# Kernel optimization log

Measured on AMD Instinct MI355X. Metric: run time of the kernel, lower is better.

The kernel has to match this reference:

```python
import jax, jax.numpy as jnp
import numpy as np

EPS = 1e-5

def _conv1x1(x, W, b):
    # x: [B,Ci,H,W], W: [Co,Ci]
    return jnp.einsum('oi,bihw->bohw', W, x) + b[None, :, None, None]

def _bn(x, gamma, beta, mean, var):
    # inference-mode BatchNorm2d
    s = gamma / jnp.sqrt(var + EPS)
    return x * s[None, :, None, None] + (beta - mean * s)[None, :, None, None]

def _conv3x3(x, W, b):
    y = jax.lax.conv_general_dilated(x, W, (1, 1), 'SAME',
                                     dimension_numbers=('NCHW', 'OIHW', 'NCHW'))
    return y + b[None, :, None, None]

def _sparsemax_last(S):
    # sparsemax over the last axis (TrackHSPA: max-subtract, sort, cumsum, threshold)
    S = S - jnp.max(S, axis=-1, keepdims=True)
    srt = -jnp.sort(-S, axis=-1)                 # descending sort
    csum = jnp.cumsum(srt, axis=-1) - 1.0
    N = S.shape[-1]
    ar = jnp.arange(1, N + 1, dtype=S.dtype)
    mask = ar * srt > csum
    k = jnp.sum(mask, axis=-1, keepdims=True)    # support size per row
    tau = jnp.take_along_axis(csum, k - 1, axis=-1) / k.astype(S.dtype)
    return jnp.maximum(S - tau, 0.0)

def _forward(zf, xf, Wq, bq, Ws, bs, Wg, bg, g_gamma, g_beta, g_mean, g_var,
             Wfi, bfi, fi_gamma, fi_beta, fi_mean, fi_var,
             Wm, bm, m_gamma, m_beta, m_mean, m_var, prelu_a):
    B, C, Hx, Wx = xf.shape
    # ---- Graph_Attention_Union (cross-attention) ----
    xf_t = _conv1x1(xf, Wq, bq).reshape(B, C, -1)      # [B,C,Nx]
    zf_t = _conv1x1(zf, Ws, bs).reshape(B, C, -1)      # [B,C,Nz]
    xf_g = jax.nn.relu(_bn(_conv1x1(xf, Wg, bg), g_gamma, g_beta, g_mean, g_var))
    zf_g = jax.nn.relu(_bn(_conv1x1(zf, Wg, bg), g_gamma, g_beta, g_mean, g_var))
    sim = jnp.einsum('bcn,bcm->bnm', xf_t, zf_t)       # [B,Nx,Nz]
    attn = jax.nn.softmax(sim, axis=2)
    emb = jnp.einsum('bcm,bnm->bcn', zf_g.reshape(B, C, -1), attn)
    emb = emb.reshape(B, C, Hx, Wx)
    gat = jax.nn.relu(_bn(_conv1x1(jnp.concatenate([emb, xf_g], axis=1), Wfi, bfi),
                          fi_gamma, fi_beta, fi_mean, fi_var))
    # ---- TrackHSPA (adaptive sparsemax self-attention) ----
    e = _conv3x3(gat, Wm, bm)
    e = _bn(e, m_gamma, m_beta, m_mean, m_var)
    e = jnp.where(e >= 0, e, prelu_a * e)              # PReLU (single param)
    N = Hx * Wx
    ef = e.reshape(B, -1, N)                           # [B,C',N]
    S = jnp.einsum('bdi,bdj->bij', ef, ef)             # [B,N,N]
    P = _sparsemax_last(S)
    out = jnp.einsum('bcn,bnm->bcm', gat.reshape(B, C, N), P)
    return out.reshape(B, C, Hx, Wx) + gat


def setup_inputs():
    key = jax.random.key(0)
    ks = jax.random.split(key, 8)
    B, C, Hz, Wz, Hx, Wx = 32, 256, 7, 7, 31, 31
    Cm = C // 4
    f = lambda k, shape: jax.random.normal(k, shape, jnp.float32) * 0.05
    return {
        'zf': jax.random.normal(ks[0], (B, C, Hz, Wz), jnp.float32),
        'xf': jax.random.normal(ks[1], (B, C, Hx, Wx), jnp.float32),
        'Wq': f(ks[2], (C, C)), 'bq': jnp.zeros((C,), jnp.float32),
        'Ws': f(ks[3], (C, C)), 'bs': jnp.zeros((C,), jnp.float32),
        'Wg': f(ks[4], (C, C)), 'bg': jnp.zeros((C,), jnp.float32),
        'g_gamma': jnp.ones((C,), jnp.float32), 'g_beta': jnp.zeros((C,), jnp.float32),
        'g_mean': jnp.zeros((C,), jnp.float32), 'g_var': jnp.ones((C,), jnp.float32),
        'Wfi': f(ks[5], (C, 2 * C)), 'bfi': jnp.zeros((C,), jnp.float32),
        'fi_gamma': jnp.ones((C,), jnp.float32), 'fi_beta': jnp.zeros((C,), jnp.float32),
        'fi_mean': jnp.zeros((C,), jnp.float32), 'fi_var': jnp.ones((C,), jnp.float32),
        'Wm': f(ks[6], (Cm, C, 3, 3)), 'bm': jnp.zeros((Cm,), jnp.float32),
        'm_gamma': jnp.ones((Cm,), jnp.float32), 'm_beta': jnp.zeros((Cm,), jnp.float32),
        'm_mean': jnp.zeros((Cm,), jnp.float32), 'm_var': jnp.ones((Cm,), jnp.float32),
        'prelu_a': jnp.array(0.25, jnp.float32),
    }


def reference(zf, xf, Wq, bq, Ws, bs, Wg, bg, g_gamma, g_beta, g_mean, g_var,
              Wfi, bfi, fi_gamma, fi_beta, fi_mean, fi_var,
              Wm, bm, m_gamma, m_beta, m_mean, m_var, prelu_a):
    return _forward(zf, xf, Wq, bq, Ws, bs, Wg, bg, g_gamma, g_beta, g_mean, g_var,
                    Wfi, bfi, fi_gamma, fi_beta, fi_mean, fi_var,
                    Wm, bm, m_gamma, m_beta, m_mean, m_var, prelu_a)
```

## Files before the change

### kernel.cpp

```cpp
#include <hip/hip_runtime.h>
#include <cstdint>
#include <cstddef>
#include <math.h>

typedef __attribute__((ext_vector_type(8))) short short8;
typedef __attribute__((ext_vector_type(4))) float floatx4;
typedef unsigned short ushort_t;

__device__ __forceinline__ ushort_t f2bf(float x) {
    union { float f; unsigned u; } v; v.f = x;
    unsigned r = v.u + 0x7FFF + ((v.u >> 16) & 1);
    return (ushort_t)(r >> 16);
}
__device__ __forceinline__ float bf2f(ushort_t h) {
    union { unsigned u; float f; } v; v.u = ((unsigned)h) << 16; return v.f;
}
__device__ __forceinline__ void split2(float v, ushort_t& h, ushort_t& l) {
    h = f2bf(v);
    l = f2bf(v - bf2f(h));
}

#define MFMA(a, b, c) __builtin_amdgcn_mfma_f32_16x16x32_bf16((a), (b), (c), 0, 0, 0)

__global__ void prep_all_kernel(
    const float* __restrict__ Wq, const float* __restrict__ Ws,
    const float* __restrict__ Wg, const float* __restrict__ Wfi,
    const float* __restrict__ Wm,
    const float* bq, const float* bs,
    const float* bg, const float* gg, const float* gb, const float* gm, const float* gv,
    const float* bfi, const float* fg, const float* fb, const float* fm, const float* fv,
    const float* bm, const float* mg, const float* mb, const float* mm, const float* mv,
    ushort_t* Wq_h, ushort_t* Wq_l, ushort_t* Ws_h, ushort_t* Ws_l,
    ushort_t* Wg_h, ushort_t* Wg_l, ushort_t* Wfi_h, ushort_t* Wfi_l,
    ushort_t* wm_h, ushort_t* wm_l, float* scsh)
{
    int bid = blockIdx.x, t = threadIdx.x;
    if (bid < 256) {
        int i = bid * 256 + t; ushort_t h, l; split2(Wq[i], h, l); Wq_h[i] = h; Wq_l[i] = l;
    } else if (bid < 512) {
        int i = (bid - 256) * 256 + t; ushort_t h, l; split2(Ws[i], h, l); Ws_h[i] = h; Ws_l[i] = l;
    } else if (bid < 768) {
        int i = (bid - 512) * 256 + t; ushort_t h, l; split2(Wg[i], h, l); Wg_h[i] = h; Wg_l[i] = l;
    } else if (bid < 1280) {
        int i = (bid - 768) * 256 + t; ushort_t h, l; split2(Wfi[i], h, l); Wfi_h[i] = h; Wfi_l[i] = l;
    } else if (bid < 1856) {
        int i = (bid - 1280) * 256 + t;
        int c = i & 255, m = (i >> 8) & 63, tap = i >> 14;
        ushort_t h, l; split2(Wm[((size_t)m * 256 + c) * 9 + tap], h, l);
        wm_h[i] = h; wm_l[i] = l;
    } else {
        if (t < 256) {
            scsh[t] = 1.f;        scsh[256 + t] = bq[t];
            scsh[512 + t] = 1.f;  scsh[768 + t] = bs[t];
            float s = gg[t] * rsqrtf(gv[t] + 1e-5f);
            scsh[1024 + t] = s;   scsh[1280 + t] = gb[t] + s * (bg[t] - gm[t]);
            float s2 = fg[t] * rsqrtf(fv[t] + 1e-5f);
            scsh[1536 + t] = s2;  scsh[1792 + t] = fb[t] + s2 * (bfi[t] - fm[t]);
            if (t < 64) {
                float s3 = mg[t] * rsqrtf(mv[t] + 1e-5f);
                scsh[2048 + t] = s3; scsh[2112 + t] = mb[t] + s3 * (bm[t] - mm[t]);
            }
        }
    }
}

__global__ void halo_zero_kernel(ushort_t* __restrict__ gxh, ushort_t* __restrict__ gxl) {
    int i = blockIdx.x * 256 + threadIdx.x;
    int b = i >> 7, k = i & 127;
    int r;
    if (k < 33) r = k;
    else if (k < 66) r = 32 * 33 + (k - 33);
    else { int k2 = k - 66; r = ((k2 >> 1) + 1) * 33 + ((k2 & 1) ? 32 : 0); }
    uint4* ph = (uint4*)(gxh + ((size_t)b * 1089 + r) * 256);
    uint4* pl = (uint4*)(gxl + ((size_t)b * 1089 + r) * 256);
    uint4 z = make_uint4(0, 0, 0, 0);
#pragma unroll
    for (int s = 0; s < 32; s++) { ph[s] = z; pl[s] = z; }
}

__global__ __launch_bounds__(256) void transpose_in_kernel(
    const float* __restrict__ in, ushort_t* __restrict__ oh, ushort_t* __restrict__ ol,
    int Nsrc, int Npad)
{
    int b = blockIdx.z;
    const float* ib = in + (size_t)b * 256 * Nsrc;
    ushort_t* obh = oh + (size_t)b * Npad * 256;
    ushort_t* obl = ol + (size_t)b * Npad * 256;
    __shared__ float tile[32][33];
    int n0 = blockIdx.x * 32, c0 = blockIdx.y * 32;
    int tx = threadIdx.x & 31, ty = threadIdx.x >> 5;
#pragma unroll
    for (int r = 0; r < 4; r++) {
        int c = c0 + ty + r * 8, n = n0 + tx;
        tile[ty + r * 8][tx] = (n < Nsrc) ? ib[(size_t)c * Nsrc + n] : 0.f;
    }
    __syncthreads();
#pragma unroll
    for (int r = 0; r < 4; r++) {
        int n = n0 + ty + r * 8, c = c0 + tx;
        if (n < Nsrc) {
            ushort_t h, l; split2(tile[tx][ty + r * 8], h, l);
            obh[(size_t)n * 256 + c] = h;
            obl[(size_t)n * 256 + c] = l;
        }
    }
}

__global__ __launch_bounds__(256) void dualconv_mfma_kernel(
    const ushort_t* __restrict__ Xh, const ushort_t* __restrict__ Xl,
    const ushort_t* __restrict__ W1h, const ushort_t* __restrict__ W1l,
    const ushort_t* __restrict__ W2h, const ushort_t* __restrict__ W2l,
    const float* __restrict__ sc1, const float* __restrict__ sh1,
    const float* __restrict__ sc2, const float* __restrict__ sh2,
    int relu1, int relu2,
    ushort_t* __restrict__ O1h, ushort_t* __restrict__ O1l,
    ushort_t* __restrict__ O2h, ushort_t* __restrict__ O2l,
    ushort_t* __restrict__ O2ch, ushort_t* __restrict__ O2cl, int cpitch,
    int K, int Nvalid, int NpadIn, int NpadOut)
{
    int b = blockIdx.x;
    int half = blockIdx.y & 1;
    int n0 = (blockIdx.y >> 1) * 64;
    const ushort_t* Xbh = Xh + (size_t)b * NpadIn * K;
    const ushort_t* Xbl = Xl + (size_t)b * NpadIn * K;
    int tid = threadIdx.x, w = tid >> 6, l = tid & 63, lc = l & 15, q = l >> 4;
    int m0 = w * 64;

    const ushort_t* Wh = half ? W2h : W1h;
    const ushort_t* Wl = half ? W2l : W1l;
    const float* sc = half ? sc2 : sc1;
    const float* sh = half ? sh2 : sh1;
    int relu = half ? relu2 : relu1;
    ushort_t* Obh = (half ? O2h : O1h) + (size_t)b * NpadOut * 256;
    ushort_t* Obl = (half ? O2l : O1l) + (size_t)b * NpadOut * 256;

    int nrow[4];
#pragma unroll
    for (int jt = 0; jt < 4; jt++) {
        int nr = n0 + jt * 16 + lc;
        nrow[jt] = (nr < NpadIn) ? nr : (NpadIn - 1);
    }

    floatx4 acc[4][4];
#pragma unroll
    for (int i = 0; i < 4; i++)
#pragma unroll
        for (int j = 0; j < 4; j++) acc[i][j] = (floatx4){0.f, 0.f, 0.f, 0.f};

    for (int k0 = 0; k0 < K; k0 += 32) {
        short8 ah[4], al[4], bh[4], bl[4];
#pragma unroll
        for (int mt = 0; mt < 4; mt++) {
            size_t off = (size_t)(m0 + mt * 16 + lc) * K + k0 + q * 8;
            ah[mt] = *(const short8*)(Wh + off);
            al[mt] = *(const short8*)(Wl + off);
        }
#pragma unroll
        for (int jt = 0; jt < 4; jt++) {
            size_t off = (size_t)nrow[jt] * K + k0 + q * 8;
            bh[jt] = *(const short8*)(Xbh + off);
            bl[jt] = *(const short8*)(Xbl + off);
        }
#pragma unroll
        for (int mt = 0; mt < 4; mt++)
#pragma unroll
            for (int jt = 0; jt < 4; jt++) {
                acc[mt][jt] = MFMA(ah[mt], bh[jt], acc[mt][jt]);
                acc[mt][jt] = MFMA(ah[mt], bl[jt], acc[mt][jt]);
                acc[mt][jt] = MFMA(al[mt], bh[jt], acc[mt][jt]);
            }
    }
#pragma unroll
    for (int mt = 0; mt < 4; mt++) {
        int mb = m0 + mt * 16 + q * 4;
        float s0 = sc[mb], s1 = sc[mb + 1], s2 = sc[mb + 2], s3 = sc[mb + 3];
        float h0 = sh[mb], h1 = sh[mb + 1], h2 = sh[mb + 2], h3 = sh[mb + 3];
#pragma unroll
        for (int jt = 0; jt < 4; jt++) {
            int n = n0 + jt * 16 + lc;
            if (n >= Nvalid) continue;
            float v0 = acc[mt][jt][0] * s0 + h0;
            float v1 = acc[mt][jt][1] * s1 + h1;
            float v2 = acc[mt][jt][2] * s2 + h2;
            float v3 = acc[mt][jt][3] * s3 + h3;
            if (relu) { v0 = fmaxf(v0, 0.f); v1 = fmaxf(v1, 0.f); v2 = fmaxf(v2, 0.f); v3 = fmaxf(v3, 0.f); }
            ushort_t e0, f0, e1, f1, e2, f2, e3, f3;
            split2(v0, e0, f0); split2(v1, e1, f1); split2(v2, e2, f2); split2(v3, e3, f3);
            *(ushort4*)(Obh + (size_t)n * 256 + mb) = make_ushort4(e0, e1, e2, e3);
            *(ushort4*)(Obl + (size_t)n * 256 + mb) = make_ushort4(f0, f1, f2, f3);
            if (half && O2ch) {
                O2ch[((size_t)b * 256 + mb + 0) * cpitch + n] = e0;
                O2ch[((size_t)b * 256 + mb + 1) * cpitch + n] = e1;
                O2ch[((size_t)b * 256 + mb + 2) * cpitch + n] = e2;
                O2ch[((size_t)b * 256 + mb + 3) * cpitch + n] = e3;
                O2cl[((size_t)b * 256 + mb + 0) * cpitch + n] = f0;
                O2cl[((size_t)b * 256 + mb + 1) * cpitch + n] = f1;
                O2cl[((size_t)b * 256 + mb + 2) * cpitch + n] = f2;
                O2cl[((size_t)b * 256 + mb + 3) * cpitch + n] = f3;
            }
        }
    }
}

__global__ __launch_bounds__(256) void attn_mfma_kernel(
    const ushort_t* __restrict__ xth, const ushort_t* __restrict__ xtl,
    const ushort_t* __restrict__ zth, const ushort_t* __restrict__ ztl,
    const ushort_t* __restrict__ zgh, const ushort_t* __restrict__ zgl,
    ushort_t* __restrict__ eh, ushort_t* __restrict__ el)
{
    __shared__ float S[64][68];
    __shared__ ushort_t awh[64][72], awl[64][72];
    __shared__ float T[4][16][20];
    int b = blockIdx.x, n0 = blockIdx.y * 64;
    int tid = threadIdx.x, w = tid >> 6, l = tid & 63, lc = l & 15, q = l >> 4;
    const ushort_t* xhb = xth + (size_t)b * 992 * 256;
    const ushort_t* xlb = xtl + (size_t)b * 992 * 256;
    const ushort_t* zhb = zth + (size_t)b * 64 * 256;
    const ushort_t* zlb = ztl + (size_t)b * 64 * 256;
    const ushort_t* ghb = zgh + (size_t)b * 256 * 64;
    const ushort_t* glb = zgl + (size_t)b * 256 * 64;

    int rowg = n0 + w * 16 + lc;
#pragma unroll
    for (int ct = 0; ct < 4; ct++) {
        floatx4 acc = (floatx4){0.f, 0.f, 0.f, 0.f};
        for (int k0 = 0; k0 < 256; k0 += 32) {
            short8 ah = *(const short8*)(xhb + (size_t)rowg * 256 + k0 + q * 8);
            short8 al = *(const short8*)(xlb + (size_t)rowg * 256 + k0 + q * 8);
            short8 bh = *(const short8*)(zhb + (size_t)(ct * 16 + lc) * 256 + k0 + q * 8);
            short8 bl = *(const short8*)(zlb + (size_t)(ct * 16 + lc) * 256 + k0 + q * 8);
            acc = MFMA(ah, bh, acc);
            acc = MFMA(ah, bl, acc);
            acc = MFMA(al, bh, acc);
        }
#pragma unroll
        for (int r = 0; r < 4; r++) S[w * 16 + q * 4 + r][ct * 16 + lc] = acc[r];
    }
    __syncthreads();
    if (tid < 64) {
        float mx = -INFINITY;
        for (int m = 0; m < 49; m++) mx = fmaxf(mx, S[tid][m]);
        float sum = 0.f;
        for (int m = 0; m < 49; m++) { float e = __expf(S[tid][m] - mx); S[tid][m] = e; sum += e; }
        float inv = 1.f / sum;
        for (int m = 0; m < 64; m++) {
            float vv = (m < 49) ? S[tid][m] * inv : 0.f;
            ushort_t hh, ll; split2(vv, hh, ll);
            awh[tid][m] = hh; awl[tid][m] = ll;
        }
    }
    __syncthreads();
    int nw = l >> 2, cg = l & 3;
#pragma unroll
    for (int ct = 0; ct < 16; ct++) {
        floatx4 acc = (floatx4){0.f, 0.f, 0.f, 0.f};
#pragma unroll
        for (int k0 = 0; k0 < 64; k0 += 32) {
            short8 ah = *(const short8*)(&awh[w * 16 + lc][k0 + q * 8]);
            short8 al = *(const short8*)(&awl[w * 16 + lc][k0 + q * 8]);
            short8 bh = *(const short8*)(ghb + (size_t)(ct * 16 + lc) * 64 + k0 + q * 8);
            short8 bl = *(const short8*)(glb + (size_t)(ct * 16 + lc) * 64 + k0 + q * 8);
            acc = MFMA(ah, bh, acc);
            acc = MFMA(ah, bl, acc);
            acc = MFMA(al, bh, acc);
        }
#pragma unroll
        for (int r = 0; r < 4; r++) T[w][q * 4 + r][lc] = acc[r];
        float4 vv = *(const float4*)&T[w][nw][cg * 4];
        int n = n0 + w * 16 + nw;
        if (n < 961) {
            ushort_t h0, l0, h1, l1, h2, l2_, h3, l3;
            split2(vv.x, h0, l0); split2(vv.y, h1, l1);
            split2(vv.z, h2, l2_); split2(vv.w, h3, l3);
            size_t off = ((size_t)b * 992 + n) * 256 + ct * 16 + cg * 4;
            *(ushort4*)(eh + off) = make_ushort4(h0, h1, h2, h3);
            *(ushort4*)(el + off) = make_ushort4(l0, l1, l2_, l3);
        }
    }
}

__global__ __launch_bounds__(256) void fi_mfma_kernel(
    const ushort_t* __restrict__ Eh, const ushort_t* __restrict__ El,
    const ushort_t* __restrict__ Gh, const ushort_t* __restrict__ Gl,
    const ushort_t* __restrict__ Wh, const ushort_t* __restrict__ Wl,
    const float* __restrict__ sc, const float* __restrict__ sh,
    ushort_t* __restrict__ gxh, ushort_t* __restrict__ gxl,
    ushort_t* __restrict__ gat_nf)
{
    int b = blockIdx.x;
    const ushort_t* Ebh = Eh + (size_t)b * 992 * 256;
    const ushort_t* Ebl = El + (size_t)b * 992 * 256;
    const ushort_t* Gbh = Gh + (size_t)b * 992 * 256;
    const ushort_t* Gbl = Gl + (size_t)b * 992 * 256;
    ushort_t* gxhb = gxh + (size_t)b * 1089 * 256;
    ushort_t* gxlb = gxl + (size_t)b * 1089 * 256;
    ushort_t* gn = gat_nf + (size_t)b * 256 * 992;
    int tid = threadIdx.x, w = tid >> 6, l = tid & 63, lc = l & 15, q = l >> 4;
    int m0 = w * 64, nb0 = blockIdx.y * 32;

    floatx4 acc[4][2];
#pragma unroll
    for (int i = 0; i < 4; i++)
#pragma unroll
        for (int j = 0; j < 2; j++) acc[i][j] = (floatx4){0.f, 0.f, 0.f, 0.f};

    for (int k0 = 0; k0 < 512; k0 += 32) {
        const ushort_t* sh_ = (k0 < 256) ? Ebh : Gbh;
        const ushort_t* sl_ = (k0 < 256) ? Ebl : Gbl;
        int kk = (k0 < 256) ? k0 : k0 - 256;
        short8 ah[4], al[4], bh[2], bl[2];
#pragma unroll
        for (int mt = 0; mt < 4; mt++) {
            size_t off = (size_t)(m0 + mt * 16 + lc) * 512 + k0 + q * 8;
            ah[mt] = *(const short8*)(Wh + off);
            al[mt] = *(const short8*)(Wl + off);
        }
#pragma unroll
        for (int jt = 0; jt < 2; jt++) {
            size_t off = (size_t)(nb0 + jt * 16 + lc) * 256 + kk + q * 8;
            bh[jt] = *(const short8*)(sh_ + off);
            bl[jt] = *(const short8*)(sl_ + off);
        }
#pragma unroll
        for (int mt = 0; mt < 4; mt++)
#pragma unroll
            for (int jt = 0; jt < 2; jt++) {
                acc[mt][jt] = MFMA(ah[mt], bh[jt], acc[mt][jt]);
                acc[mt][jt] = MFMA(ah[mt], bl[jt], acc[mt][jt]);
                acc[mt][jt] = MFMA(al[mt], bh[jt], acc[mt][jt]);
            }
    }
#pragma unroll
    for (int mt = 0; mt < 4; mt++) {
        int mb = m0 + mt * 16 + q * 4;
        float s0 = sc[mb], s1 = sc[mb + 1], s2 = sc[mb + 2], s3 = sc[mb + 3];
        float h0 = sh[mb], h1 = sh[mb + 1], h2 = sh[mb + 2], h3 = sh[mb + 3];
#pragma unroll
        for (int jt = 0; jt < 2; jt++) {
            int n = nb0 + jt * 16 + lc;
            if (n >= 961) continue;
            float v0 = fmaxf(acc[mt][jt][0] * s0 + h0, 0.f);
            float v1 = fmaxf(acc[mt][jt][1] * s1 + h1, 0.f);
            float v2 = fmaxf(acc[mt][jt][2] * s2 + h2, 0.f);
            float v3 = fmaxf(acc[mt][jt][3] * s3 + h3, 0.f);
            ushort_t a0, b0, a1, b1, a2, b2, a3, b3;
            split2(v0, a0, b0); split2(v1, a1, b1); split2(v2, a2, b2); split2(v3, a3, b3);
            int hh = n / 31, ww2 = n - hh * 31;
            int row = (hh + 1) * 33 + (ww2 + 1);
            *(ushort4*)(gxhb + (size_t)row * 256 + mb) = make_ushort4(a0, a1, a2, a3);
            *(ushort4*)(gxlb + (size_t)row * 256 + mb) = make_ushort4(b0, b1, b2, b3);
            gn[(size_t)(mb + 0) * 992 + n] = a0;
            gn[(size_t)(mb + 1) * 992 + n] = a1;
            gn[(size_t)(mb + 2) * 992 + n] = a2;
            gn[(size_t)(mb + 3) * 992 + n] = a3;
        }
    }
}

__global__ __launch_bounds__(256) void conv3x3_mfma_kernel(
    const ushort_t* __restrict__ gxh, const ushort_t* __restrict__ gxl,
    const ushort_t* __restrict__ wmh, const ushort_t* __restrict__ wml,
    const float* __restrict__ sc, const float* __restrict__ sh,
    const float* __restrict__ prelu_a,
    ushort_t* __restrict__ eh, ushort_t* __restrict__ el)
{
    __shared__ float Sp[4][2048];
    int b = blockIdx.x;
    const ushort_t* gxhb = gxh + (size_t)b * 1089 * 256;
    const ushort_t* gxlb = gxl + (size_t)b * 1089 * 256;
    ushort_t* ebh = eh + (size_t)b * 1024 * 64;
    ushort_t* ebl = el + (size_t)b * 1024 * 64;
    int tid = threadIdx.x, w = tid >> 6, l = tid & 63, lc = l & 15, q = l >> 4;
    int j0 = blockIdx.y * 32;

    int base[2];
#pragma unroll
    for (int jt = 0; jt < 2; jt++) {
        int j = j0 + jt * 16 + lc; if (j > 960) j = 960;
        int hh = j / 31, ww2 = j - hh * 31;
        base[jt] = (hh + 1) * 33 + (ww2 + 1);
    }

    floatx4 acc[4][2];
#pragma unroll
    for (int i = 0; i < 4; i++)
#pragma unroll
        for (int j = 0; j < 2; j++) acc[i][j] = (floatx4){0.f, 0.f, 0.f, 0.f};

    for (int s = w * 18; s < w * 18 + 18; s++) {
        int tap = s >> 3, k0 = (s & 7) * 32;
        int doff = (tap / 3 - 1) * 33 + (tap % 3 - 1);
        const ushort_t* wth = wmh + tap * 16384;
        const ushort_t* wtl = wml + tap * 16384;
        short8 ah[4], al_[4], bh[2], bl[2];
#pragma unroll
        for (int mt = 0; mt < 4; mt++) {
            size_t off = (size_t)(mt * 16 + lc) * 256 + k0 + q * 8;
            ah[mt]  = *(const short8*)(wth + off);
            al_[mt] = *(const short8*)(wtl + off);
        }
#pragma unroll
        for (int jt = 0; jt < 2; jt++) {
            size_t off = (size_t)(base[jt] + doff) * 256 + k0 + q * 8;
            bh[jt] = *(const short8*)(gxhb + off);
            bl[jt] = *(const short8*)(gxlb + off);
        }
#pragma unroll
        for (int mt = 0; mt < 4; mt++)
#pragma unroll
            for (int jt = 0; jt < 2; jt++) {
                acc[mt][jt] = MFMA(ah[mt], bh[jt], acc[mt][jt]);
                acc[mt][jt] = MFMA(ah[mt], bl[jt], acc[mt][jt]);
                acc[mt][jt] = MFMA(al_[mt], bh[jt], acc[mt][jt]);
            }
    }

#pragma unroll
    for (int mt = 0; mt < 4; mt++)
#pragma unroll
        for (int jt = 0; jt < 2; jt++)
#pragma unroll
            for (int r = 0; r < 4; r++)
                Sp[w][(mt * 16 + q * 4 + r) * 32 + jt * 16 + lc] = acc[mt][jt][r];
    __syncthreads();

    float pa = prelu_a[0];
#pragma unroll
    for (int gi = 0; gi < 2; gi++) {
        int g = tid + gi * 256;
        int j = g & 31, mg = g >> 5;
        int m = mg * 4;
        int jj = j0 + j;
        if (jj >= 961) continue;
        float v[4];
#pragma unroll
        for (int i = 0; i < 4; i++) {
            int idx = (m + i) * 32 + j;
            v[i] = Sp[0][idx] + Sp[1][idx] + Sp[2][idx] + Sp[3][idx];
            v[i] = v[i] * sc[m + i] + sh[m + i];
            v[i] = v[i] >= 0.f ? v[i] : pa * v[i];
        }
        ushort_t a0, b0, a1, b1, a2, b2, a3, b3;
        split2(v[0], a0, b0); split2(v[1], a1, b1);
        split2(v[2], a2, b2); split2(v[3], a3, b3);
        *(ushort4*)(ebh + (size_t)jj * 64 + m) = make_ushort4(a0, a1, a2, a3);
        *(ushort4*)(ebl + (size_t)jj * 64 + m) = make_ushort4(b0, b1, b2, b3);
    }
}

__global__ __launch_bounds__(512) void hspa_mfma_kernel(
    const ushort_t* __restrict__ eh, const ushort_t* __restrict__ el,
    ushort_t* __restrict__ PT)
{
    const int PITCH = 978;
    __shared__ float S[16 * 978];
    int b = blockIdx.x, nb = blockIdx.y;
    const ushort_t* ebh = eh + (size_t)b * 1024 * 64;
    const ushort_t* ebl = el + (size_t)b * 1024 * 64;
    ushort_t* Pb = PT + (size_t)b * 1024 * 992;
    int tid = threadIdx.x, w = tid >> 6, l = tid & 63, lc = l & 15, q = l >> 4;
    int n0 = nb * 16;

    short8 a0h = *(const short8*)(ebh + (size_t)(n0 + lc) * 64 + q * 8);
    short8 a0l = *(const short8*)(ebl + (size_t)(n0 + lc) * 64 + q * 8);
    short8 a1h = *(const short8*)(ebh + (size_t)(n0 + lc) * 64 + 32 + q * 8);
    short8 a1l = *(const short8*)(ebl + (size_t)(n0 + lc) * 64 + 32 + q * 8);

    for (int jt = w; jt < 61; jt += 8) {
        int j = jt * 16 + lc;
        short8 b0h = *(const short8*)(ebh + (size_t)j * 64 + q * 8);
        short8 b0l = *(const short8*)(ebl + (size_t)j * 64 + q * 8);
        short8 b1h = *(const short8*)(ebh + (size_t)j * 64 + 32 + q * 8);
        short8 b1l = *(const short8*)(ebl + (size_t)j * 64 + 32 + q * 8);
        floatx4 acc = (floatx4){0.f, 0.f, 0.f, 0.f};
        acc = MFMA(a0h, b0h, acc);
        acc = MFMA(a0h, b0l, acc);
        acc = MFMA(a0l, b0h, acc);
        acc = MFMA(a1h, b1h, acc);
        acc = MFMA(a1h, b1l, acc);
        acc = MFMA(a1l, b1h, acc);
#pragma unroll
        for (int r = 0; r < 4; r++) S[(q * 4 + r) * PITCH + j] = acc[r];
    }
    __syncthreads();

    int r0 = w * 2, r1 = w * 2 + 1;
    float sv0[16], sv1[16];
    float mx0 = -INFINITY, mx1 = -INFINITY;
#pragma unroll
    for (int t = 0; t < 16; t++) {
        int j = l + t * 64;
        float s0 = (j < 961) ? S[r0 * PITCH + j] : -INFINITY;
        float s1 = (j < 961) ? S[r1 * PITCH + j] : -INFINITY;
        sv0[t] = s0; sv1[t] = s1;
        mx0 = fmaxf(mx0, s0); mx1 = fmaxf(mx1, s1);
    }
    for (int off = 32; off; off >>= 1) {
        mx0 = fmaxf(mx0, __shfl_xor(mx0, off));
        mx1 = fmaxf(mx1, __shfl_xor(mx1, off));
    }
#pragma unroll
    for (int t = 0; t < 16; t++) { sv0[t] -= mx0; sv1[t] -= mx1; }

    float tau0 = -1.f, tau1 = -1.f;
    for (int it = 0; it < 16; it++) {
        float s0 = 0.f, c0 = 0.f, s1 = 0.f, c1 = 0.f;
#pragma unroll
        for (int t = 0; t < 16; t++) {
            if (sv0[t] > tau0) { s0 += sv0[t]; c0 += 1.f; }
            if (sv1[t] > tau1) { s1 += sv1[t]; c1 += 1.f; }
        }
        for (int off = 32; off; off >>= 1) {
            s0 += __shfl_xor(s0, off); c0 += __shfl_xor(c0, off);
            s1 += __shfl_xor(s1, off); c1 += __shfl_xor(c1, off);
        }
        float nt0 = (s0 - 1.f) / c0;
        float nt1 = (s1 - 1.f) / c1;
        bool conv = (nt0 == tau0) && (nt1 == tau1);
        tau0 = nt0; tau1 = nt1;
        if (conv) break;
    }
#pragma unroll
    for (int t = 0; t < 16; t++) {
        int j = l + t * 64;
        if (j < 976) {
            S[r0 * PITCH + j] = (j < 961) ? fmaxf(sv0[t] - tau0, 0.f) : 0.f;
            S[r1 * PITCH + j] = (j < 961) ? fmaxf(sv1[t] - tau1, 0.f) : 0.f;
        }
    }
    __syncthreads();

    for (int j = tid; j < 976; j += 512) {
        union { ushort_t u[8]; uint4 v; } p0, p1;
#pragma unroll
        for (int r = 0; r < 8; r++)  p0.u[r] = f2bf(S[r * PITCH + j]);
#pragma unroll
        for (int r = 0; r < 8; r++)  p1.u[r] = f2bf(S[(8 + r) * PITCH + j]);
        ushort_t* dst = Pb + (size_t)j * 992 + n0;
        *(uint4*)(dst) = p0.v;
        *(uint4*)(dst + 8) = p1.v;
    }
}

__global__ __launch_bounds__(256) void out_mfma_kernel(
    const ushort_t* __restrict__ gat_nf, const ushort_t* __restrict__ PT,
    float* __restrict__ out)
{
    int b = blockIdx.x, jb = blockIdx.y;
    const ushort_t* gb = gat_nf + (size_t)b * 256 * 992;
    const ushort_t* Pb = PT + (size_t)b * 1024 * 992;
    float* ob = out + (size_t)b * 256 * 961;
    int tid = threadIdx.x, w = tid >> 6, l = tid & 63, lc = l & 15, q = l >> 4;
    int m0 = w * 64, j0 = jb * 64;

    floatx4 acc[4][4];
#pragma unroll
    for (int i = 0; i < 4; i++)
#pragma unroll
        for (int j = 0; j < 4; j++) acc[i][j] = (floatx4){0.f, 0.f, 0.f, 0.f};

    for (int k0 = 0; k0 < 992; k0 += 32) {
        short8 a[4], bb[4];
#pragma unroll
        for (int mt = 0; mt < 4; mt++)
            a[mt] = *(const short8*)(gb + (size_t)(m0 + mt * 16 + lc) * 992 + k0 + q * 8);
#pragma unroll
        for (int jt = 0; jt < 4; jt++)
            bb[jt] = *(const short8*)(Pb + (size_t)(j0 + jt * 16 + lc) * 992 + k0 + q * 8);
#pragma unroll
        for (int mt = 0; mt < 4; mt++)
#pragma unroll
            for (int jt = 0; jt < 4; jt++)
                acc[mt][jt] = MFMA(a[mt], bb[jt], acc[mt][jt]);
    }
#pragma unroll
    for (int mt = 0; mt < 4; mt++) {
        int mb = m0 + mt * 16 + q * 4;
#pragma unroll
        for (int jt = 0; jt < 4; jt++) {
            int j = j0 + jt * 16 + lc;
            if (j >= 961) continue;
#pragma unroll
            for (int r = 0; r < 4; r++) {
                float g = bf2f(gb[(size_t)(mb + r) * 992 + j]);
                ob[(size_t)(mb + r) * 961 + j] = acc[mt][jt][r] + g;
            }
        }
    }
}

extern "C" void kernel_launch(void* const* d_in, const int* in_sizes, int n_in,
                              void* d_out, int out_size, void* d_ws, size_t ws_size,
                              hipStream_t stream)
{
    const float* zf      = (const float*)d_in[0];
    const float* xf      = (const float*)d_in[1];
    const float* Wq      = (const float*)d_in[2];
    const float* bq      = (const float*)d_in[3];
    const float* Ws      = (const float*)d_in[4];
    const float* bs      = (const float*)d_in[5];
    const float* Wg      = (const float*)d_in[6];
    const float* bg      = (const float*)d_in[7];
    const float* g_gamma = (const float*)d_in[8];
    const float* g_beta  = (const float*)d_in[9];
    const float* g_mean  = (const float*)d_in[10];
    const float* g_var   = (const float*)d_in[11];
    const float* Wfi     = (const float*)d_in[12];
    const float* bfi     = (const float*)d_in[13];
    const float* fi_gamma= (const float*)d_in[14];
    const float* fi_beta = (const float*)d_in[15];
    const float* fi_mean = (const float*)d_in[16];
    const float* fi_var  = (const float*)d_in[17];
    const float* Wm      = (const float*)d_in[18];
    const float* bm      = (const float*)d_in[19];
    const float* m_gamma = (const float*)d_in[20];
    const float* m_beta  = (const float*)d_in[21];
    const float* m_mean  = (const float*)d_in[22];
    const float* m_var   = (const float*)d_in[23];
    const float* prelu_a = (const float*)d_in[24];
    float* out = (float*)d_out;

    ushort_t* ws = (ushort_t*)d_ws;
    ushort_t* Wq_h  = ws + 0;         ushort_t* Wq_l  = ws + 65536;
    ushort_t* Ws_h  = ws + 131072;    ushort_t* Ws_l  = ws + 196608;
    ushort_t* Wg_h  = ws + 262144;    ushort_t* Wg_l  = ws + 327680;
    ushort_t* Wfi_h = ws + 393216;    ushort_t* Wfi_l = ws + 524288;
    ushort_t* wm_h  = ws + 655360;    ushort_t* wm_l  = ws + 802816;
    ushort_t* XT_h    = ws + 950272;
    ushort_t* XT_l    = ws + 9076736;
    ushort_t* xf_tT_h = ws + 17203200;
    ushort_t* xf_tT_l = ws + 25329664;
    ushort_t* zf_tT_h = ws + 33456128;
    ushort_t* zf_tT_l = ws + 33980416;
    ushort_t* zf_gT_h = ws + 34504704;
    ushort_t* zf_gT_l = ws + 35028992;
    ushort_t* gxT_h   = ws + 17203200;
    ushort_t* gxT_l   = ws + 26124288;
    ushort_t* xf_gT_h = ws + 35553280;
    ushort_t* xf_gT_l = ws + 43679744;
    ushort_t* gat_nf  = ws + 51806208;
    ushort_t* eT_h    = ws + 59932672;
    ushort_t* eT_l    = ws + 62029824;
    ushort_t* PT      = ws + 64126976;
    ushort_t* zfT_h   = ws + 96632832;
    ushort_t* zfT_l   = ws + 97157120;
    float* scsh       = (float*)(ws + 97681408);
    ushort_t* zgC_h   = ws + 97685760;
    ushort_t* zgC_l   = ws + 98210048;
    ushort_t* embT_h = XT_h;
    ushort_t* embT_l = XT_l;

    const float* sc_q  = scsh + 0,    *sh_q  = scsh + 256;
    const float* sc_s  = scsh + 512,  *sh_s  = scsh + 768;
    const float* sc_g  = scsh + 1024, *sh_g  = scsh + 1280;
    const float* sc_fi = scsh + 1536, *sh_fi = scsh + 1792;
    const float* sc_m  = scsh + 2048, *sh_m  = scsh + 2112;

    prep_all_kernel<<<1857, 256, 0, stream>>>(
        Wq, Ws, Wg, Wfi, Wm,
        bq, bs, bg, g_gamma, g_beta, g_mean, g_var,
        bfi, fi_gamma, fi_beta, fi_mean, fi_var,
        bm, m_gamma, m_beta, m_mean, m_var,
        Wq_h, Wq_l, Ws_h, Ws_l, Wg_h, Wg_l, Wfi_h, Wfi_l, wm_h, wm_l, scsh);

    transpose_in_kernel<<<dim3(31, 8, 32), 256, 0, stream>>>(xf, XT_h, XT_l, 961, 992);
    transpose_in_kernel<<<dim3(2, 8, 32), 256, 0, stream>>>(zf, zfT_h, zfT_l, 49, 64);

    dualconv_mfma_kernel<<<dim3(32, 32), 256, 0, stream>>>(
        XT_h, XT_l, Wq_h, Wq_l, Wg_h, Wg_l,
        sc_q, sh_q, sc_g, sh_g, 0, 1,
        xf_tT_h, xf_tT_l, xf_gT_h, xf_gT_l,
        nullptr, nullptr, 0, 256, 961, 992, 992);
    dualconv_mfma_kernel<<<dim3(32, 2), 256, 0, stream>>>(
        zfT_h, zfT_l, Ws_h, Ws_l, Wg_h, Wg_l,
        sc_s, sh_s, sc_g, sh_g, 0, 1,
        zf_tT_h, zf_tT_l, zf_gT_h, zf_gT_l,
        zgC_h, zgC_l, 64, 256, 49, 64, 64);

    attn_mfma_kernel<<<dim3(32, 16), 256, 0, stream>>>(
        xf_tT_h, xf_tT_l, zf_tT_h, zf_tT_l, zgC_h, zgC_l, embT_h, embT_l);

    halo_zero_kernel<<<16, 256, 0, stream>>>(gxT_h, gxT_l);

    fi_mfma_kernel<<<dim3(32, 31), 256, 0, stream>>>(
        embT_h, embT_l, xf_gT_h, xf_gT_l, Wfi_h, Wfi_l, sc_fi, sh_fi,
        gxT_h, gxT_l, gat_nf);

    conv3x3_mfma_kernel<<<dim3(32, 31), 256, 0, stream>>>(
        gxT_h, gxT_l, wm_h, wm_l, sc_m, sh_m, prelu_a, eT_h, eT_l);

    hspa_mfma_kernel<<<dim3(32, 61), 512, 0, stream>>>(eT_h, eT_l, PT);

    out_mfma_kernel<<<dim3(32, 16), 256, 0, stream>>>(gat_nf, PT, out);
}
```

Baseline: 643.1 us.

## Double-buffer register loads in MFMA GEMM loops and widen conv3x3 tiles

Adds software pipelining (double-buffered register prefetch of the next K slice) to the dualconv, fi, conv3x3 and out MFMA kernels, so global loads overlap with MFMA work. The conv3x3 kernel now covers 64 output positions per block instead of 32, with a two-phase shared-memory reduction epilogue, and its grid is halved. Launch bounds hint at two blocks per SIMD. In exchange, register pressure rises, which could cause spills, and fewer blocks may reduce occupancy.

```diff
diff --git a/kernel.cpp b/kernel.cpp
--- a/kernel.cpp
+++ b/kernel.cpp
@@ -106,7 +106,7 @@
     }
 }
 
-__global__ __launch_bounds__(256) void dualconv_mfma_kernel(
+__global__ __launch_bounds__(256, 2) void dualconv_mfma_kernel(
     const ushort_t* __restrict__ Xh, const ushort_t* __restrict__ Xl,
     const ushort_t* __restrict__ W1h, const ushort_t* __restrict__ W1l,
     const ushort_t* __restrict__ W2h, const ushort_t* __restrict__ W2l,
@@ -147,29 +147,51 @@
 #pragma unroll
         for (int j = 0; j < 4; j++) acc[i][j] = (floatx4){0.f, 0.f, 0.f, 0.f};
 
-    for (int k0 = 0; k0 < K; k0 += 32) {
-        short8 ah[4], al[4], bh[4], bl[4];
-#pragma unroll
-        for (int mt = 0; mt < 4; mt++) {
-            size_t off = (size_t)(m0 + mt * 16 + lc) * K + k0 + q * 8;
-            ah[mt] = *(const short8*)(Wh + off);
-            al[mt] = *(const short8*)(Wl + off);
-        }
-#pragma unroll
-        for (int jt = 0; jt < 4; jt++) {
-            size_t off = (size_t)nrow[jt] * K + k0 + q * 8;
-            bh[jt] = *(const short8*)(Xbh + off);
-            bl[jt] = *(const short8*)(Xbl + off);
-        }
-#pragma unroll
-        for (int mt = 0; mt < 4; mt++)
-#pragma unroll
-            for (int jt = 0; jt < 4; jt++) {
-                acc[mt][jt] = MFMA(ah[mt], bh[jt], acc[mt][jt]);
-                acc[mt][jt] = MFMA(ah[mt], bl[jt], acc[mt][jt]);
-                acc[mt][jt] = MFMA(al[mt], bh[jt], acc[mt][jt]);
-            }
-    }
+#define DC_LOADA(K0, AH, AL) do { \
+    _Pragma("unroll") \
+    for (int mt_ = 0; mt_ < 4; mt_++) { \
+        size_t off_ = (size_t)(m0 + mt_ * 16 + lc) * K + (K0) + q * 8; \
+        AH[mt_] = *(const short8*)(Wh + off_); \
+        AL[mt_] = *(const short8*)(Wl + off_); \
+    } \
+} while (0)
+#define DC_LOADB(K0, BH, BL) do { \
+    _Pragma("unroll") \
+    for (int jt_ = 0; jt_ < 4; jt_++) { \
+        size_t off_ = (size_t)nrow[jt_] * K + (K0) + q * 8; \
+        BH[jt_] = *(const short8*)(Xbh + off_); \
+        BL[jt_] = *(const short8*)(Xbl + off_); \
+    } \
+} while (0)
+#define DC_MFMA(AH, AL, BH, BL) do { \
+    _Pragma("unroll") \
+    for (int mt_ = 0; mt_ < 4; mt_++) \
+    _Pragma("unroll") \
+    for (int jt_ = 0; jt_ < 4; jt_++) { \
+        acc[mt_][jt_] = MFMA(AH[mt_], BH[jt_], acc[mt_][jt_]); \
+        acc[mt_][jt_] = MFMA(AH[mt_], BL[jt_], acc[mt_][jt_]); \
+        acc[mt_][jt_] = MFMA(AL[mt_], BH[jt_], acc[mt_][jt_]); \
+    } \
+} while (0)
+
+    short8 ah0[4], al0[4], bh0[4], bl0[4];
+    short8 ah1[4], al1[4], bh1[4], bl1[4];
+    DC_LOADA(0, ah0, al0);
+    DC_LOADB(0, bh0, bl0);
+    for (int k0 = 0; k0 < K; k0 += 64) {
+        DC_LOADA(k0 + 32, ah1, al1);
+        DC_LOADB(k0 + 32, bh1, bl1);
+        DC_MFMA(ah0, al0, bh0, bl0);
+        if (k0 + 64 < K) {
+            DC_LOADA(k0 + 64, ah0, al0);
+            DC_LOADB(k0 + 64, bh0, bl0);
+        }
+        DC_MFMA(ah1, al1, bh1, bl1);
+    }
+#undef DC_LOADA
+#undef DC_LOADB
+#undef DC_MFMA
+
 #pragma unroll
     for (int mt = 0; mt < 4; mt++) {
         int mb = m0 + mt * 16 + q * 4;
@@ -304,32 +326,52 @@
 #pragma unroll
         for (int j = 0; j < 2; j++) acc[i][j] = (floatx4){0.f, 0.f, 0.f, 0.f};
 
-    for (int k0 = 0; k0 < 512; k0 += 32) {
-        const ushort_t* sh_ = (k0 < 256) ? Ebh : Gbh;
-        const ushort_t* sl_ = (k0 < 256) ? Ebl : Gbl;
-        int kk = (k0 < 256) ? k0 : k0 - 256;
-        short8 ah[4], al[4], bh[2], bl[2];
+#define FI_LOADB(K0, BH, BL) do { \
+    const ushort_t* sh__ = ((K0) < 256) ? Ebh : Gbh; \
+    const ushort_t* sl__ = ((K0) < 256) ? Ebl : Gbl; \
+    int kk_ = ((K0) < 256) ? (K0) : (K0) - 256; \
+    _Pragma("unroll") \
+    for (int jt_ = 0; jt_ < 2; jt_++) { \
+        size_t off_ = (size_t)(nb0 + jt_ * 16 + lc) * 256 + kk_ + q * 8; \
+        BH[jt_] = *(const short8*)(sh__ + off_); \
+        BL[jt_] = *(const short8*)(sl__ + off_); \
+    } \
+} while (0)
+#define FI_MFMA(BH, BL) do { \
+    _Pragma("unroll") \
+    for (int mt_ = 0; mt_ < 4; mt_++) \
+    _Pragma("unroll") \
+    for (int jt_ = 0; jt_ < 2; jt_++) { \
+        acc[mt_][jt_] = MFMA(ah[mt_], BH[jt_], acc[mt_][jt_]); \
+        acc[mt_][jt_] = MFMA(ah[mt_], BL[jt_], acc[mt_][jt_]); \
+        acc[mt_][jt_] = MFMA(al[mt_], BH[jt_], acc[mt_][jt_]); \
+    } \
+} while (0)
+
+    short8 bh0[2], bl0[2], bh1[2], bl1[2];
+    FI_LOADB(0, bh0, bl0);
+    for (int k0 = 0; k0 < 512; k0 += 64) {
+        short8 ah[4], al[4];
 #pragma unroll
         for (int mt = 0; mt < 4; mt++) {
             size_t off = (size_t)(m0 + mt * 16 + lc) * 512 + k0 + q * 8;
             ah[mt] = *(const short8*)(Wh + off);
             al[mt] = *(const short8*)(Wl + off);
         }
-#pragma unroll
-        for (int jt = 0; jt < 2; jt++) {
-            size_t off = (size_t)(nb0 + jt * 16 + lc) * 256 + kk + q * 8;
-            bh[jt] = *(const short8*)(sh_ + off);
-            bl[jt] = *(const short8*)(sl_ + off);
-        }
-#pragma unroll
-        for (int mt = 0; mt < 4; mt++)
-#pragma unroll
-            for (int jt = 0; jt < 2; jt++) {
-                acc[mt][jt] = MFMA(ah[mt], bh[jt], acc[mt][jt]);
-                acc[mt][jt] = MFMA(ah[mt], bl[jt], acc[mt][jt]);
-                acc[mt][jt] = MFMA(al[mt], bh[jt], acc[mt][jt]);
-            }
-    }
+        FI_LOADB(k0 + 32, bh1, bl1);
+        FI_MFMA(bh0, bl0);
+#pragma unroll
+        for (int mt = 0; mt < 4; mt++) {
+            size_t off = (size_t)(m0 + mt * 16 + lc) * 512 + k0 + 32 + q * 8;
+            ah[mt] = *(const short8*)(Wh + off);
+            al[mt] = *(const short8*)(Wl + off);
+        }
+        if (k0 + 64 < 512) FI_LOADB(k0 + 64, bh0, bl0);
+        FI_MFMA(bh1, bl1);
+    }
+#undef FI_LOADB
+#undef FI_MFMA
+
 #pragma unroll
     for (int mt = 0; mt < 4; mt++) {
         int mb = m0 + mt * 16 + q * 4;
@@ -357,7 +399,7 @@
     }
 }
 
-__global__ __launch_bounds__(256) void conv3x3_mfma_kernel(
+__global__ __launch_bounds__(256, 2) void conv3x3_mfma_kernel(
     const ushort_t* __restrict__ gxh, const ushort_t* __restrict__ gxl,
     const ushort_t* __restrict__ wmh, const ushort_t* __restrict__ wml,
     const float* __restrict__ sc, const float* __restrict__ sh,
@@ -371,80 +413,99 @@
     ushort_t* ebh = eh + (size_t)b * 1024 * 64;
     ushort_t* ebl = el + (size_t)b * 1024 * 64;
     int tid = threadIdx.x, w = tid >> 6, l = tid & 63, lc = l & 15, q = l >> 4;
-    int j0 = blockIdx.y * 32;
-
-    int base[2];
-#pragma unroll
-    for (int jt = 0; jt < 2; jt++) {
+    int j0 = blockIdx.y * 64;
+
+    int base[4];
+#pragma unroll
+    for (int jt = 0; jt < 4; jt++) {
         int j = j0 + jt * 16 + lc; if (j > 960) j = 960;
         int hh = j / 31, ww2 = j - hh * 31;
         base[jt] = (hh + 1) * 33 + (ww2 + 1);
     }
 
-    floatx4 acc[4][2];
+    floatx4 acc[4][4];
 #pragma unroll
     for (int i = 0; i < 4; i++)
 #pragma unroll
-        for (int j = 0; j < 2; j++) acc[i][j] = (floatx4){0.f, 0.f, 0.f, 0.f};
-
-    for (int s = w * 18; s < w * 18 + 18; s++) {
-        int tap = s >> 3, k0 = (s & 7) * 32;
-        int doff = (tap / 3 - 1) * 33 + (tap % 3 - 1);
-        const ushort_t* wth = wmh + tap * 16384;
-        const ushort_t* wtl = wml + tap * 16384;
-        short8 ah[4], al_[4], bh[2], bl[2];
-#pragma unroll
-        for (int mt = 0; mt < 4; mt++) {
-            size_t off = (size_t)(mt * 16 + lc) * 256 + k0 + q * 8;
-            ah[mt]  = *(const short8*)(wth + off);
-            al_[mt] = *(const short8*)(wtl + off);
-        }
-#pragma unroll
-        for (int jt = 0; jt < 2; jt++) {
-            size_t off = (size_t)(base[jt] + doff) * 256 + k0 + q * 8;
-            bh[jt] = *(const short8*)(gxhb + off);
-            bl[jt] = *(const short8*)(gxlb + off);
-        }
+        for (int j = 0; j < 4; j++) acc[i][j] = (floatx4){0.f, 0.f, 0.f, 0.f};
+
+#define C3_LOAD(SL, AH, AL, BH, BL) do { \
+    int sl_ = (SL); \
+    int tap_ = (sl_ >= 9) ? sl_ - 9 : sl_; \
+    int k0_ = (w * 2 + ((sl_ >= 9) ? 1 : 0)) * 32; \
+    int doff_ = (tap_ / 3 - 1) * 33 + (tap_ % 3 - 1); \
+    const ushort_t* wth_ = wmh + tap_ * 16384; \
+    const ushort_t* wtl_ = wml + tap_ * 16384; \
+    _Pragma("unroll") \
+    for (int mt_ = 0; mt_ < 4; mt_++) { \
+        size_t off_ = (size_t)(mt_ * 16 + lc) * 256 + k0_ + q * 8; \
+        AH[mt_] = *(const short8*)(wth_ + off_); \
+        AL[mt_] = *(const short8*)(wtl_ + off_); \
+    } \
+    _Pragma("unroll") \
+    for (int jt_ = 0; jt_ < 4; jt_++) { \
+        size_t off_ = (size_t)(base[jt_] + doff_) * 256 + k0_ + q * 8; \
+        BH[jt_] = *(const short8*)(gxhb + off_); \
+        BL[jt_] = *(const short8*)(gxlb + off_); \
+    } \
+} while (0)
+#define C3_MFMA(AH, AL, BH, BL) do { \
+    _Pragma("unroll") \
+    for (int mt_ = 0; mt_ < 4; mt_++) \
+    _Pragma("unroll") \
+    for (int jt_ = 0; jt_ < 4; jt_++) { \
+        acc[mt_][jt_] = MFMA(AH[mt_], BH[jt_], acc[mt_][jt_]); \
+        acc[mt_][jt_] = MFMA(AH[mt_], BL[jt_], acc[mt_][jt_]); \
+        acc[mt_][jt_] = MFMA(AL[mt_], BH[jt_], acc[mt_][jt_]); \
+    } \
+} while (0)
+
+    short8 A0h[4], A0l[4], B0h[4], B0l[4];
+    short8 A1h[4], A1l[4], B1h[4], B1l[4];
+    C3_LOAD(0, A0h, A0l, B0h, B0l);
+#pragma unroll
+    for (int it = 0; it < 9; it++) {
+        C3_LOAD(it * 2 + 1, A1h, A1l, B1h, B1l);
+        C3_MFMA(A0h, A0l, B0h, B0l);
+        if (it < 8) C3_LOAD(it * 2 + 2, A0h, A0l, B0h, B0l);
+        C3_MFMA(A1h, A1l, B1h, B1l);
+    }
+#undef C3_LOAD
+#undef C3_MFMA
+
+    float pa = prelu_a[0];
+#pragma unroll
+    for (int ph = 0; ph < 2; ph++) {
+        __syncthreads();
 #pragma unroll
         for (int mt = 0; mt < 4; mt++)
 #pragma unroll
-            for (int jt = 0; jt < 2; jt++) {
-                acc[mt][jt] = MFMA(ah[mt], bh[jt], acc[mt][jt]);
-                acc[mt][jt] = MFMA(ah[mt], bl[jt], acc[mt][jt]);
-                acc[mt][jt] = MFMA(al_[mt], bh[jt], acc[mt][jt]);
+            for (int jt = 0; jt < 2; jt++)
+#pragma unroll
+                for (int r = 0; r < 4; r++)
+                    Sp[w][(mt * 16 + q * 4 + r) * 32 + jt * 16 + lc] = acc[mt][ph * 2 + jt][r];
+        __syncthreads();
+#pragma unroll
+        for (int gi = 0; gi < 2; gi++) {
+            int g = tid + gi * 256;
+            int j = g & 31, mg = g >> 5;
+            int m = mg * 4;
+            int jj = j0 + ph * 32 + j;
+            if (jj >= 961) continue;
+            float v[4];
+#pragma unroll
+            for (int i = 0; i < 4; i++) {
+                int idx = (m + i) * 32 + j;
+                v[i] = Sp[0][idx] + Sp[1][idx] + Sp[2][idx] + Sp[3][idx];
+                v[i] = v[i] * sc[m + i] + sh[m + i];
+                v[i] = v[i] >= 0.f ? v[i] : pa * v[i];
             }
-    }
-
-#pragma unroll
-    for (int mt = 0; mt < 4; mt++)
-#pragma unroll
-        for (int jt = 0; jt < 2; jt++)
-#pragma unroll
-            for (int r = 0; r < 4; r++)
-                Sp[w][(mt * 16 + q * 4 + r) * 32 + jt * 16 + lc] = acc[mt][jt][r];
-    __syncthreads();
-
-    float pa = prelu_a[0];
-#pragma unroll
-    for (int gi = 0; gi < 2; gi++) {
-        int g = tid + gi * 256;
-        int j = g & 31, mg = g >> 5;
-        int m = mg * 4;
-        int jj = j0 + j;
-        if (jj >= 961) continue;
-        float v[4];
-#pragma unroll
-        for (int i = 0; i < 4; i++) {
-            int idx = (m + i) * 32 + j;
-            v[i] = Sp[0][idx] + Sp[1][idx] + Sp[2][idx] + Sp[3][idx];
-            v[i] = v[i] * sc[m + i] + sh[m + i];
-            v[i] = v[i] >= 0.f ? v[i] : pa * v[i];
-        }
-        ushort_t a0, b0, a1, b1, a2, b2, a3, b3;
-        split2(v[0], a0, b0); split2(v[1], a1, b1);
-        split2(v[2], a2, b2); split2(v[3], a3, b3);
-        *(ushort4*)(ebh + (size_t)jj * 64 + m) = make_ushort4(a0, a1, a2, a3);
-        *(ushort4*)(ebl + (size_t)jj * 64 + m) = make_ushort4(b0, b1, b2, b3);
+            ushort_t a0, b0, a1, b1, a2, b2, a3, b3;
+            split2(v[0], a0, b0); split2(v[1], a1, b1);
+            split2(v[2], a2, b2); split2(v[3], a3, b3);
+            *(ushort4*)(ebh + (size_t)jj * 64 + m) = make_ushort4(a0, a1, a2, a3);
+            *(ushort4*)(ebl + (size_t)jj * 64 + m) = make_ushort4(b0, b1, b2, b3);
+        }
     }
 }
 
@@ -542,7 +603,7 @@
     }
 }
 
-__global__ __launch_bounds__(256) void out_mfma_kernel(
+__global__ __launch_bounds__(256, 2) void out_mfma_kernel(
     const ushort_t* __restrict__ gat_nf, const ushort_t* __restrict__ PT,
     float* __restrict__ out)
 {
@@ -559,20 +620,34 @@
 #pragma unroll
         for (int j = 0; j < 4; j++) acc[i][j] = (floatx4){0.f, 0.f, 0.f, 0.f};
 
-    for (int k0 = 0; k0 < 992; k0 += 32) {
-        short8 a[4], bb[4];
-#pragma unroll
-        for (int mt = 0; mt < 4; mt++)
-            a[mt] = *(const short8*)(gb + (size_t)(m0 + mt * 16 + lc) * 992 + k0 + q * 8);
-#pragma unroll
-        for (int jt = 0; jt < 4; jt++)
-            bb[jt] = *(const short8*)(Pb + (size_t)(j0 + jt * 16 + lc) * 992 + k0 + q * 8);
-#pragma unroll
-        for (int mt = 0; mt < 4; mt++)
-#pragma unroll
-            for (int jt = 0; jt < 4; jt++)
-                acc[mt][jt] = MFMA(a[mt], bb[jt], acc[mt][jt]);
-    }
+#define OUT_LOAD(K0, AA, BB) do { \
+    _Pragma("unroll") \
+    for (int mt_ = 0; mt_ < 4; mt_++) \
+        AA[mt_] = *(const short8*)(gb + (size_t)(m0 + mt_ * 16 + lc) * 992 + (K0) + q * 8); \
+    _Pragma("unroll") \
+    for (int jt_ = 0; jt_ < 4; jt_++) \
+        BB[jt_] = *(const short8*)(Pb + (size_t)(j0 + jt_ * 16 + lc) * 992 + (K0) + q * 8); \
+} while (0)
+#define OUT_MFMA(AA, BB) do { \
+    _Pragma("unroll") \
+    for (int mt_ = 0; mt_ < 4; mt_++) \
+    _Pragma("unroll") \
+    for (int jt_ = 0; jt_ < 4; jt_++) \
+        acc[mt_][jt_] = MFMA(AA[mt_], BB[jt_], acc[mt_][jt_]); \
+} while (0)
+
+    short8 a0[4], b0[4], a1[4], b1[4];
+    OUT_LOAD(0, a0, b0);
+    for (int k0 = 0; k0 < 960; k0 += 64) {
+        OUT_LOAD(k0 + 32, a1, b1);
+        OUT_MFMA(a0, b0);
+        OUT_LOAD(k0 + 64, a0, b0);
+        OUT_MFMA(a1, b1);
+    }
+    OUT_MFMA(a0, b0);
+#undef OUT_LOAD
+#undef OUT_MFMA
+
 #pragma unroll
     for (int mt = 0; mt < 4; mt++) {
         int mb = m0 + mt * 16 + q * 4;
@@ -686,7 +761,7 @@
         embT_h, embT_l, xf_gT_h, xf_gT_l, Wfi_h, Wfi_l, sc_fi, sh_fi,
         gxT_h, gxT_l, gat_nf);
 
-    conv3x3_mfma_kernel<<<dim3(32, 31), 256, 0, stream>>>(
+    conv3x3_mfma_kernel<<<dim3(32, 16), 256, 0, stream>>>(
         gxT_h, gxT_l, wm_h, wm_l, sc_m, sh_m, prelu_a, eT_h, eT_l);
 
     hspa_mfma_kernel<<<dim3(32, 61), 512, 0, stream>>>(eT_h, eT_l, PT);
```

After: 608.2 us. -5.4%, faster.
